# Kernel tuning notes

Hardware: AMD Instinct MI355X
Metric: run time of the kernel (lower is better)

Reference implementation:

```python
import jax, jax.numpy as jnp
import numpy as np

BN_EPS = 1e-3  # keras BatchNormalization default epsilon


def setup_inputs() -> dict:
    key = jax.random.key(0)
    k1, k2, k3 = jax.random.split(key, 3)
    B, H, W, C, K = 16, 32, 32, 256, 32
    support = 1.0 / (K * C) ** 0.5
    inputs = jax.random.normal(k1, (B, H, W, C), dtype=jnp.float32)
    codewords = jax.random.uniform(k2, (1, 1, K, C), minval=-support, maxval=support, dtype=jnp.float32)
    smoothing_factors = jax.random.uniform(k3, (1, 1, K), minval=-1.0, maxval=0.0, dtype=jnp.float32)
    gamma = jnp.ones((C,), dtype=jnp.float32)
    beta = jnp.zeros((C,), dtype=jnp.float32)
    return {"inputs": inputs, "codewords": codewords, "smoothing_factors": smoothing_factors,
            "gamma": gamma, "beta": beta}


def reference(inputs, codewords, smoothing_factors, gamma, beta):
    B, H, W, C = inputs.shape
    n = H * W
    feats = inputs.reshape(B, n, 1, C)
    # residuals: [B, n, K, C]
    residuals = feats - codewords
    # squared norms over features -> [B, n, K]
    sqnorms = jnp.sum(residuals * residuals, axis=-1)
    # smoothed softmax over codewords
    w = jax.nn.softmax(sqnorms * smoothing_factors, axis=-1)  # [B, n, K]
    # softmax-weighted residual sum over spatial positions -> [B, K, C]
    enc = jnp.einsum('bnk,bnkc->bkc', w, residuals)
    # BatchNorm over last axis (training-mode batch stats over axes (0,1))
    mean = jnp.mean(enc, axis=(0, 1))
    var = jnp.var(enc, axis=(0, 1))
    bn = (enc - mean) * jax.lax.rsqrt(var + BN_EPS) * gamma + beta
    # ReLU then sum over codewords -> [B, C]
    return jnp.sum(jax.nn.relu(bn), axis=1)
```

## Files before the change

kernel.cpp:

```cpp
#include <hip/hip_runtime.h>
#include <hip/hip_bf16.h>


#define BN_EPS 1e-3f

typedef __attribute__((ext_vector_type(8))) short short8;
typedef __attribute__((ext_vector_type(4))) float f32x4;

static __device__ inline unsigned short f2bf(float f) {
    unsigned int u = __float_as_uint(f);
    unsigned int r = (u + 0x7fffu + ((u >> 16) & 1u)) >> 16;
    return (unsigned short)r;
}

static __device__ inline short8 pack8(float4 u, float4 v) {
    short8 r;
    r[0] = (short)f2bf(u.x); r[1] = (short)f2bf(u.y);
    r[2] = (short)f2bf(u.z); r[3] = (short)f2bf(u.w);
    r[4] = (short)f2bf(v.x); r[5] = (short)f2bf(v.y);
    r[6] = (short)f2bf(v.z); r[7] = (short)f2bf(v.w);
    return r;
}

#if __has_builtin(__builtin_amdgcn_global_load_lds)
#define HAVE_GLOAD_LDS 1
typedef const __attribute__((address_space(1))) void* as1_cvp;
typedef __attribute__((address_space(3))) void* as3_vp;
static __device__ inline void gload_lds16(const void* g, void* s) {
    __builtin_amdgcn_global_load_lds((as1_cvp)g, (as3_vp)s, 16, 0, 0);
}
#else
#define HAVE_GLOAD_LDS 0
#endif

__global__ __launch_bounds__(512, 1) void enc_main_mfma(
    const float* __restrict__ x, const float* __restrict__ cw,
    const float* __restrict__ sf, float* __restrict__ pS1, float* __restrict__ pW)
{
    const int bid = blockIdx.x;
    const int b   = bid >> 4;
    const int jb2 = bid & 15;
    const int t = threadIdx.x;
    const int w = t >> 6;
    const int lane = t & 63;
    const int mt   = w >> 2;
    const int half = (w >> 1) & 1;
    const int dup  = w & 1;
    const int lrow = lane & 15;
    const int g    = lane >> 4;

    __shared__ float4 xs4[32][65];
    __shared__ unsigned short cwbf[32][264];
    __shared__ float  ccred[16][32];
    __shared__ float4 dred[2][2][2][2][64];
    __shared__ float  xxr[2][2][2][16];
    __shared__ unsigned short xbf[32][264];
    __shared__ unsigned short wT[32][40];
    __shared__ float  w_lds[2][32][33];
    __shared__ float  cc_lds[32];
    __shared__ float  sf_lds[32];

    const float4* gx4 = (const float4*)(x + (size_t)b * 1024 * 256)
                        + (size_t)jb2 * 64 * 64;

#if HAVE_GLOAD_LDS
    #pragma unroll
    for (int i = 0; i < 4; ++i) {
        const int row = w * 4 + i;
        gload_lds16(gx4 + row * 64 + lane, &xs4[row][0]);
    }
#else
    {
        const int p = t >> 4, q = t & 15;
        #pragma unroll
        for (int j = 0; j < 4; ++j)
            xs4[p][q + 16 * j] = gx4[p * 64 + q + 16 * j];
    }
#endif
    {
        const int k = t >> 4, seg = t & 15;
        const float4* cw4 = (const float4*)cw;
        float s = 0.f;
        #pragma unroll
        for (int jj = 0; jj < 2; ++jj) {
            float4 u0 = cw4[k * 64 + seg * 4 + 2 * jj];
            float4 u1 = cw4[k * 64 + seg * 4 + 2 * jj + 1];
            s += u0.x * u0.x + u0.y * u0.y + u0.z * u0.z + u0.w * u0.w
               + u1.x * u1.x + u1.y * u1.y + u1.z * u1.z + u1.w * u1.w;
            *(short8*)&cwbf[k][seg * 16 + 8 * jj] = pack8(u0, u1);
        }
        ccred[seg][k] = s;
    }
    if (t < 32) sf_lds[t] = sf[t];
    __syncthreads();

    if (t < 32) {
        float s = 0.f;
        #pragma unroll
        for (int j = 0; j < 16; ++j) s += ccred[j][t];
        cc_lds[t] = s;
    }

    f32x4 E00 = {0,0,0,0}, E01 = {0,0,0,0}, E10 = {0,0,0,0}, E11 = {0,0,0,0};
    const float* xsf = (const float*)xs4;

    #pragma unroll
    for (int tile = 0; tile < 2; ++tile) {
        f32x4 D0 = {0,0,0,0}, D1 = {0,0,0,0};
        float xxp = 0.f;
        #pragma unroll
        for (int k2 = 0; k2 < 2; ++k2) {
            const int ks = dup * 2 + k2;
            const int ch = half * 128 + ks * 32 + g * 8;
            const int row = mt * 16 + lrow;
            const float* ap = xsf + row * 260 + ch;
            float4 uu = *(const float4*)ap;
            float4 vv = *(const float4*)(ap + 4);
            xxp += uu.x * uu.x + uu.y * uu.y + uu.z * uu.z + uu.w * uu.w
                 + vv.x * vv.x + vv.y * vv.y + vv.z * vv.z + vv.w * vv.w;
            short8 a = pack8(uu, vv);
            *(short8*)&xbf[row][ch] = a;
            short8 b0 = *(const short8*)&cwbf[lrow][ch];
            short8 b1 = *(const short8*)&cwbf[16 + lrow][ch];
            D0 = __builtin_amdgcn_mfma_f32_16x16x32_bf16(a, b0, D0, 0, 0, 0);
            D1 = __builtin_amdgcn_mfma_f32_16x16x32_bf16(a, b1, D1, 0, 0, 0);
        }
        xxp += __shfl_xor(xxp, 16, 64);
        xxp += __shfl_xor(xxp, 32, 64);
        if (lane < 16) xxr[mt][half][dup][lane] = xxp;
        dred[mt][half][dup][0][lane] = make_float4(D0[0], D0[1], D0[2], D0[3]);
        dred[mt][half][dup][1][lane] = make_float4(D1[0], D1[1], D1[2], D1[3]);
        __syncthreads();

        if (tile == 0) {
#if HAVE_GLOAD_LDS
            #pragma unroll
            for (int i = 0; i < 4; ++i) {
                const int row = w * 4 + i;
                gload_lds16(gx4 + (32 + row) * 64 + lane, &xs4[row][0]);
            }
#else
            const int p = t >> 4, q = t & 15;
            #pragma unroll
            for (int j = 0; j < 4; ++j)
                xs4[p][q + 16 * j] = gx4[(32 + p) * 64 + q + 16 * j];
#endif
        }

        {
            const int k0 = lrow, k1 = 16 + lrow;
            float d0[4], d1[4];
            #pragma unroll
            for (int nt = 0; nt < 2; ++nt) {
                float4 s00 = dred[mt][0][0][nt][lane];
                float4 s01 = dred[mt][0][1][nt][lane];
                float4 s10 = dred[mt][1][0][nt][lane];
                float4 s11 = dred[mt][1][1][nt][lane];
                float* dd = nt ? d1 : d0;
                dd[0] = s00.x + s01.x + s10.x + s11.x;
                dd[1] = s00.y + s01.y + s10.y + s11.y;
                dd[2] = s00.z + s01.z + s10.z + s11.z;
                dd[3] = s00.w + s01.w + s10.w + s11.w;
            }
            const float sf0 = sf_lds[k0], sf1 = sf_lds[k1];
            const float cc0 = cc_lds[k0], cc1 = cc_lds[k1];
            #pragma unroll
            for (int r = 0; r < 4; ++r) {
                const int pl = g * 4 + r;
                const float xxv = xxr[mt][0][0][pl] + xxr[mt][0][1][pl]
                                + xxr[mt][1][0][pl] + xxr[mt][1][1][pl];
                float s0 = sf0 * (xxv - 2.f * d0[r] + cc0);
                float s1 = sf1 * (xxv - 2.f * d1[r] + cc1);
                float m = fmaxf(s0, s1);
                #pragma unroll
                for (int msk = 1; msk <= 8; msk <<= 1) m = fmaxf(m, __shfl_xor(m, msk, 64));
                float e0 = __expf(s0 - m), e1 = __expf(s1 - m);
                float sm = e0 + e1;
                #pragma unroll
                for (int msk = 1; msk <= 8; msk <<= 1) sm += __shfl_xor(sm, msk, 64);
                const float inv = 1.f / sm;
                if (half == 0 && dup == 0) {
                    const int n = mt * 16 + pl;
                    const float w0v = e0 * inv, w1v = e1 * inv;
                    w_lds[tile][n][k0] = w0v;
                    w_lds[tile][n][k1] = w1v;
                    wT[k0][n] = f2bf(w0v);
                    wT[k1][n] = f2bf(w1v);
                }
            }
        }
        asm volatile("s_waitcnt lgkmcnt(0)" ::: "memory");
        __builtin_amdgcn_sched_barrier(0);
        __builtin_amdgcn_s_barrier();
        __builtin_amdgcn_sched_barrier(0);

        {
            short8 a0 = *(const short8*)&wT[lrow][8 * g];
            short8 a1 = *(const short8*)&wT[16 + lrow][8 * g];
            const unsigned short* xbu = &xbf[0][0];
            #pragma unroll
            for (int nt = 0; nt < 2; ++nt) {
                const int c = w * 32 + nt * 16 + lrow;
                short8 bf;
                #pragma unroll
                for (int e = 0; e < 8; ++e)
                    bf[e] = (short)xbu[(8 * g + e) * 264 + c];
                if (nt == 0) {
                    E00 = __builtin_amdgcn_mfma_f32_16x16x32_bf16(a0, bf, E00, 0, 0, 0);
                    E10 = __builtin_amdgcn_mfma_f32_16x16x32_bf16(a1, bf, E10, 0, 0, 0);
                } else {
                    E01 = __builtin_amdgcn_mfma_f32_16x16x32_bf16(a0, bf, E01, 0, 0, 0);
                    E11 = __builtin_amdgcn_mfma_f32_16x16x32_bf16(a1, bf, E11, 0, 0, 0);
                }
            }
        }
        if (tile == 0) __syncthreads();
    }

    float* dst = pS1 + (size_t)bid * 8192;
    #pragma unroll
    for (int reg = 0; reg < 4; ++reg) {
        const int k0r = (4 * g + reg) * 256;
        const int k1r = (16 + 4 * g + reg) * 256;
        dst[k0r + w * 32 +  0 + lrow] = E00[reg];
        dst[k0r + w * 32 + 16 + lrow] = E01[reg];
        dst[k1r + w * 32 +  0 + lrow] = E10[reg];
        dst[k1r + w * 32 + 16 + lrow] = E11[reg];
    }
    if (t < 32) {
        float s = 0.f;
        #pragma unroll
        for (int p = 0; p < 32; ++p) s += w_lds[0][p][t] + w_lds[1][p][t];
        pW[bid * 32 + t] = s;
    }
}

__global__ __launch_bounds__(256) void enc_reduce(
    const float* __restrict__ pS1, const float* __restrict__ pW,
    const float* __restrict__ cw, float* __restrict__ enc)
{
    const int row = blockIdx.x;
    const int b = row >> 5;
    const int k = row & 31;
    const int c = threadIdx.x;
    float s = 0.f;
    #pragma unroll
    for (int jj = 0; jj < 16; ++jj)
        s += pS1[(size_t)(b * 16 + jj) * 8192 + k * 256 + c];
    const int lane = c & 63;
    float wp = pW[(b * 16 + (lane & 15)) * 32 + k];
    #pragma unroll
    for (int m = 1; m <= 8; m <<= 1) wp += __shfl_xor(wp, m, 64);
    enc[row * 256 + c] = s - wp * cw[k * 256 + c];
}

__global__ __launch_bounds__(256) void enc_stats2(
    const float* __restrict__ enc, float* __restrict__ pst)
{
    const int p = blockIdx.x;
    const int c = threadIdx.x;
    float s = 0.f, ss = 0.f;
    #pragma unroll
    for (int r = 0; r < 8; ++r) {
        float v = enc[(p * 8 + r) * 256 + c];
        s += v;
        ss = fmaf(v, v, ss);
    }
    pst[p * 512 + c] = s;
    pst[p * 512 + 256 + c] = ss;
}

__global__ __launch_bounds__(256) void enc_out(
    const float* __restrict__ enc, const float* __restrict__ pst,
    const float* __restrict__ gamma, const float* __restrict__ beta,
    float* __restrict__ out)
{
    const int b = blockIdx.x;
    const int c = threadIdx.x;
    float S = 0.f, SS = 0.f;
    #pragma unroll 8
    for (int p = 0; p < 64; ++p) {
        S  += pst[p * 512 + c];
        SS += pst[p * 512 + 256 + c];
    }
    const float mean = S * (1.f / 512.f);
    const float var = SS * (1.f / 512.f) - mean * mean;
    const float g = gamma[c] * rsqrtf(var + BN_EPS);
    const float bt = beta[c];
    float o = 0.f;
    #pragma unroll
    for (int k = 0; k < 32; ++k) {
        float e = enc[(b * 32 + k) * 256 + c];
        float v = (e - mean) * g + bt;
        o += fmaxf(v, 0.f);
    }
    out[b * 256 + c] = o;
}

extern "C" void kernel_launch(void* const* d_in, const int* in_sizes, int n_in,
                              void* d_out, int out_size, void* d_ws, size_t ws_size,
                              hipStream_t stream) {
    const float* x     = (const float*)d_in[0];
    const float* cw    = (const float*)d_in[1];
    const float* sf    = (const float*)d_in[2];
    const float* gamma = (const float*)d_in[3];
    const float* beta  = (const float*)d_in[4];
    float* out = (float*)d_out;
    float* ws  = (float*)d_ws;

    float* pS1 = ws;
    float* pW  = pS1 + (size_t)256 * 8192;
    float* enc = pW + (size_t)256 * 32;
    float* pst = enc + (size_t)512 * 256;

    enc_main_mfma<<<256, 512, 0, stream>>>(x, cw, sf, pS1, pW);
    enc_reduce<<<512, 256, 0, stream>>>(pS1, pW, cw, enc);
    enc_stats2<<<64, 256, 0, stream>>>(enc, pst);
    enc_out<<<16, 256, 0, stream>>>(enc, pst, gamma, beta, out);
}
```

Measured before the change: 26.66 us.

## Fuse reduce, stats and output kernels into one tail kernel with atomic barriers

Merges three small post-processing kernels into a single launch. Blocks publish completion through global atomic counters, and the first 64 and then the first 16 blocks spin-wait before running the BN stats and output phases. This removes two kernel launch gaps. It relies on all 512 blocks being co-resident or scheduled in order, since otherwise the spin-waits could deadlock. Counters are reset inside the main kernel.

```diff
diff --git a/kernel.cpp b/kernel.cpp
--- a/kernel.cpp
+++ b/kernel.cpp
@@ -35,7 +35,8 @@
 
 __global__ __launch_bounds__(512, 1) void enc_main_mfma(
     const float* __restrict__ x, const float* __restrict__ cw,
-    const float* __restrict__ sf, float* __restrict__ pS1, float* __restrict__ pW)
+    const float* __restrict__ sf, float* __restrict__ pS1, float* __restrict__ pW,
+    unsigned int* __restrict__ ctrs)
 {
     const int bid = blockIdx.x;
     const int b   = bid >> 4;
@@ -48,6 +49,8 @@
     const int dup  = w & 1;
     const int lrow = lane & 15;
     const int g    = lane >> 4;
+
+    if (bid == 0 && t < 2) ctrs[t] = 0;
 
     __shared__ float4 xs4[32][65];
     __shared__ unsigned short cwbf[32][264];
@@ -235,66 +238,82 @@
     }
 }
 
-__global__ __launch_bounds__(256) void enc_reduce(
+__global__ __launch_bounds__(256) void enc_tail(
     const float* __restrict__ pS1, const float* __restrict__ pW,
-    const float* __restrict__ cw, float* __restrict__ enc)
-{
-    const int row = blockIdx.x;
-    const int b = row >> 5;
-    const int k = row & 31;
-    const int c = threadIdx.x;
-    float s = 0.f;
-    #pragma unroll
-    for (int jj = 0; jj < 16; ++jj)
-        s += pS1[(size_t)(b * 16 + jj) * 8192 + k * 256 + c];
-    const int lane = c & 63;
-    float wp = pW[(b * 16 + (lane & 15)) * 32 + k];
-    #pragma unroll
-    for (int m = 1; m <= 8; m <<= 1) wp += __shfl_xor(wp, m, 64);
-    enc[row * 256 + c] = s - wp * cw[k * 256 + c];
-}
-
-__global__ __launch_bounds__(256) void enc_stats2(
-    const float* __restrict__ enc, float* __restrict__ pst)
-{
-    const int p = blockIdx.x;
-    const int c = threadIdx.x;
-    float s = 0.f, ss = 0.f;
-    #pragma unroll
-    for (int r = 0; r < 8; ++r) {
-        float v = enc[(p * 8 + r) * 256 + c];
-        s += v;
-        ss = fmaf(v, v, ss);
-    }
-    pst[p * 512 + c] = s;
-    pst[p * 512 + 256 + c] = ss;
-}
-
-__global__ __launch_bounds__(256) void enc_out(
-    const float* __restrict__ enc, const float* __restrict__ pst,
-    const float* __restrict__ gamma, const float* __restrict__ beta,
+    const float* __restrict__ cw, const float* __restrict__ gamma,
+    const float* __restrict__ beta, float* __restrict__ enc,
+    float* __restrict__ pst, unsigned int* __restrict__ ctrs,
     float* __restrict__ out)
 {
-    const int b = blockIdx.x;
+    const int bid = blockIdx.x;
     const int c = threadIdx.x;
-    float S = 0.f, SS = 0.f;
-    #pragma unroll 8
-    for (int p = 0; p < 64; ++p) {
-        S  += pst[p * 512 + c];
-        SS += pst[p * 512 + 256 + c];
-    }
-    const float mean = S * (1.f / 512.f);
-    const float var = SS * (1.f / 512.f) - mean * mean;
-    const float g = gamma[c] * rsqrtf(var + BN_EPS);
-    const float bt = beta[c];
-    float o = 0.f;
-    #pragma unroll
-    for (int k = 0; k < 32; ++k) {
-        float e = enc[(b * 32 + k) * 256 + c];
-        float v = (e - mean) * g + bt;
-        o += fmaxf(v, 0.f);
-    }
-    out[b * 256 + c] = o;
+
+    {
+        const int b = bid >> 5, k = bid & 31;
+        float s = 0.f;
+        #pragma unroll
+        for (int jj = 0; jj < 16; ++jj)
+            s += pS1[(size_t)(b * 16 + jj) * 8192 + k * 256 + c];
+        float wp = pW[(b * 16 + (c & 15)) * 32 + k];
+        #pragma unroll
+        for (int m = 1; m <= 8; m <<= 1) wp += __shfl_xor(wp, m, 64);
+        enc[bid * 256 + c] = s - wp * cw[k * 256 + c];
+    }
+    __syncthreads();
+    if (c == 0) {
+        __threadfence();
+        __hip_atomic_fetch_add(&ctrs[0], 1u, __ATOMIC_RELEASE, __HIP_MEMORY_SCOPE_AGENT);
+    }
+    if (bid >= 64) return;
+
+    if (c == 0) {
+        while (__hip_atomic_load(&ctrs[0], __ATOMIC_ACQUIRE, __HIP_MEMORY_SCOPE_AGENT) < 512u)
+            __builtin_amdgcn_s_sleep(8);
+    }
+    __syncthreads();
+    {
+        float s = 0.f, ss = 0.f;
+        #pragma unroll
+        for (int r = 0; r < 8; ++r) {
+            float v = enc[(bid * 8 + r) * 256 + c];
+            s += v;
+            ss = fmaf(v, v, ss);
+        }
+        pst[bid * 512 + c] = s;
+        pst[bid * 512 + 256 + c] = ss;
+    }
+    __syncthreads();
+    if (c == 0) {
+        __threadfence();
+        __hip_atomic_fetch_add(&ctrs[1], 1u, __ATOMIC_RELEASE, __HIP_MEMORY_SCOPE_AGENT);
+    }
+    if (bid >= 16) return;
+
+    if (c == 0) {
+        while (__hip_atomic_load(&ctrs[1], __ATOMIC_ACQUIRE, __HIP_MEMORY_SCOPE_AGENT) < 64u)
+            __builtin_amdgcn_s_sleep(8);
+    }
+    __syncthreads();
+    {
+        float S = 0.f, SS = 0.f;
+        #pragma unroll 8
+        for (int p = 0; p < 64; ++p) {
+            S  += pst[p * 512 + c];
+            SS += pst[p * 512 + 256 + c];
+        }
+        const float mean = S * (1.f / 512.f);
+        const float var = SS * (1.f / 512.f) - mean * mean;
+        const float g = gamma[c] * rsqrtf(var + BN_EPS);
+        const float bt = beta[c];
+        float o = 0.f;
+        #pragma unroll
+        for (int k = 0; k < 32; ++k) {
+            float e = enc[(bid * 32 + k) * 256 + c];
+            float v = (e - mean) * g + bt;
+            o += fmaxf(v, 0.f);
+        }
+        out[bid * 256 + c] = o;
+    }
 }
 
 extern "C" void kernel_launch(void* const* d_in, const int* in_sizes, int n_in,
@@ -312,9 +331,8 @@
     float* pW  = pS1 + (size_t)256 * 8192;
     float* enc = pW + (size_t)256 * 32;
     float* pst = enc + (size_t)512 * 256;
-
-    enc_main_mfma<<<256, 512, 0, stream>>>(x, cw, sf, pS1, pW);
-    enc_reduce<<<512, 256, 0, stream>>>(pS1, pW, cw, enc);
-    enc_stats2<<<64, 256, 0, stream>>>(enc, pst);
-    enc_out<<<16, 256, 0, stream>>>(enc, pst, gamma, beta, out);
-}
+    unsigned int* ctrs = (unsigned int*)(pst + (size_t)64 * 512);
+
+    enc_main_mfma<<<256, 512, 0, stream>>>(x, cw, sf, pS1, pW, ctrs);
+    enc_tail<<<512, 256, 0, stream>>>(pS1, pW, cw, gamma, beta, enc, pst, ctrs, out);
+}
```

Result: slower. 49.68 us (+86.4%).
